# Performance work log

Hardware: AMD Instinct MI355X
Metric: run time of the kernel (lower is better)

Reference implementation:

```python
import jax, jax.numpy as jnp
import numpy as np

N_NODES = 100000
N_EDGES = 1000000
LATENT = 128
EMBED = 32


def setup_inputs() -> dict:
    key = jax.random.key(0)
    ks = jax.random.split(key, 10)
    z = jax.random.normal(ks[0], (N_NODES, LATENT), dtype=jnp.float32)
    edge_index = jax.random.randint(ks[1], (2, N_EDGES), 0, N_NODES, dtype=jnp.int64)
    bond_types = jax.random.randint(ks[2], (N_EDGES,), 0, 13, dtype=jnp.int64)
    d_in = 2 * LATENT + EMBED  # 288
    s = lambda k, shape, fan: jax.random.normal(k, shape, dtype=jnp.float32) / np.sqrt(fan)
    embed = s(ks[3], (13, EMBED), EMBED)
    W1 = s(ks[4], (d_in, LATENT), d_in)
    b1 = jnp.zeros((LATENT,), jnp.float32)
    W2 = s(ks[5], (LATENT, 64), LATENT)
    b2 = jnp.zeros((64,), jnp.float32)
    W3 = s(ks[6], (64, 1), 64)
    b3 = jnp.zeros((1,), jnp.float32)
    return {"z": z, "edge_index": edge_index, "bond_types": bond_types,
            "embed": embed, "W1": W1, "b1": b1, "W2": W2, "b2": b2,
            "W3": W3, "b3": b3}


def reference(z, edge_index, bond_types, embed, W1, b1, W2, b2, W3, b3):
    src, dst = edge_index[0], edge_index[1]
    # gather endpoint latents and bond-type embedding, concat -> [E, 288]
    features = jnp.concatenate([z[src], z[dst], embed[bond_types]], axis=-1)
    h = jax.nn.relu(features @ W1 + b1)   # dropout is identity in eval mode
    h = jax.nn.relu(h @ W2 + b2)
    out = jax.nn.softplus(h @ W3 + b3)
    return out.squeeze(-1)  # [E]
```

## Files before the change

kernel.cpp:

```cpp
#include <hip/hip_runtime.h>

#define E_EDGES 1000000
#define EBLK (E_EDGES / 64)
#define NNODES 100000
#define NGBLK ((NNODES + 63) / 64)
#define LATENT 128
#define DIN 288
#define H1DIM 128
#define PAD1 136
#define PAD2 66
#define PADA 296

#define WT1A 0
#define WT1B 16384
#define WT2S 32768
#define TPOFF 40960
#define UOFF 44288
#define UROWS 100032
#define VOFF (UOFF + UROWS * 128)
#define WS_SPLIT ((size_t)(VOFF + UROWS * 128) * 2)

#define MW1 0
#define MW2 36864

typedef __bf16 v8bf __attribute__((ext_vector_type(8)));
typedef __bf16 v4bf __attribute__((ext_vector_type(4)));
typedef __bf16 v2bf __attribute__((ext_vector_type(2)));
typedef float  v4f  __attribute__((ext_vector_type(4)));

__device__ __forceinline__ void cvt_store4(__bf16* p, float4 v) {
    v4bf o;
    o[0] = (__bf16)v.x; o[1] = (__bf16)v.y; o[2] = (__bf16)v.z; o[3] = (__bf16)v.w;
    *(v4bf*)p = o;
}


__global__ void prep_split(const float* __restrict__ W1, const float* __restrict__ W2,
                           const float* __restrict__ embed, const float* __restrict__ b1,
                           __bf16* __restrict__ ws) {
    int i = blockIdx.x * 256 + threadIdx.x;
    if (i < 16384) {
        int n = i >> 7, k = i & 127;
        ws[WT1A + i] = (__bf16)W1[k * 128 + n];
    } else if (i < 32768) {
        int idx = i - 16384;
        int n = idx >> 7, k = idx & 127;
        ws[WT1B + idx] = (__bf16)W1[(128 + k) * 128 + n];
    } else if (i < 40960) {
        int idx = i - 32768;
        int f = idx >> 7, k = idx & 127;
        ws[WT2S + idx] = (__bf16)W2[k * 64 + f];
    } else if (i < 40960 + 1664) {
        int idx = i - 40960;
        int b = idx >> 7, n = idx & 127;
        float s = b1[n];
        #pragma unroll
        for (int k = 0; k < 32; ++k)
            s += embed[b * 32 + k] * W1[(256 + k) * 128 + n];
        ((float*)(ws + TPOFF))[idx] = s;
    }
}

__global__ __launch_bounds__(256, 6) void node_gemm(
    const float* __restrict__ z, const __bf16* __restrict__ ws, __bf16* __restrict__ wsm)
{
    __shared__ __align__(16) __bf16 sA[64 * PAD1];
    const int tid = threadIdx.x;
    const int n0 = blockIdx.x * 64;

    {
        const int r = tid >> 2, j = tid & 3;
        int nd = n0 + r; if (nd >= NNODES) nd = NNODES - 1;
        const float4* zs = (const float4*)(z + (size_t)nd * LATENT);
        __bf16* rowp = &sA[r * PAD1];
        #pragma unroll
        for (int i = 0; i < 8; ++i) { int p = j + 4 * i; cvt_store4(rowp + p * 4, zs[p]); }
    }
    __syncthreads();

    const int wave = tid >> 6, lane = tid & 63, quad = lane >> 4, col16 = lane & 15;
    v4f zero4 = {0.f, 0.f, 0.f, 0.f};

    #pragma unroll
    for (int pass = 0; pass < 2; ++pass) {
        const __bf16* wt = ws + (pass == 0 ? WT1A : WT1B);
        __bf16* outp = wsm + (pass == 0 ? UOFF : VOFF) + (size_t)n0 * 128;
        const __bf16* w1p0 = wt + (size_t)(wave * 32 + 2 * col16) * 128;
        const __bf16* w1p1 = w1p0 + 128;
        v4f acc[4][2];
        #pragma unroll
        for (int mt = 0; mt < 4; ++mt) { acc[mt][0] = zero4; acc[mt][1] = zero4; }
        #pragma unroll
        for (int ks = 0; ks < 4; ++ks) {
            int k0 = ks * 32 + quad * 8;
            v8bf a0 = *(const v8bf*)&sA[(0 * 16 + col16) * PAD1 + k0];
            v8bf a1 = *(const v8bf*)&sA[(1 * 16 + col16) * PAD1 + k0];
            v8bf a2 = *(const v8bf*)&sA[(2 * 16 + col16) * PAD1 + k0];
            v8bf a3 = *(const v8bf*)&sA[(3 * 16 + col16) * PAD1 + k0];
            v8bf bb0 = *(const v8bf*)&w1p0[k0];
            v8bf bb1 = *(const v8bf*)&w1p1[k0];
            acc[0][0] = __builtin_amdgcn_mfma_f32_16x16x32_bf16(a0, bb0, acc[0][0], 0, 0, 0);
            acc[1][0] = __builtin_amdgcn_mfma_f32_16x16x32_bf16(a1, bb0, acc[1][0], 0, 0, 0);
            acc[2][0] = __builtin_amdgcn_mfma_f32_16x16x32_bf16(a2, bb0, acc[2][0], 0, 0, 0);
            acc[3][0] = __builtin_amdgcn_mfma_f32_16x16x32_bf16(a3, bb0, acc[3][0], 0, 0, 0);
            acc[0][1] = __builtin_amdgcn_mfma_f32_16x16x32_bf16(a0, bb1, acc[0][1], 0, 0, 0);
            acc[1][1] = __builtin_amdgcn_mfma_f32_16x16x32_bf16(a1, bb1, acc[1][1], 0, 0, 0);
            acc[2][1] = __builtin_amdgcn_mfma_f32_16x16x32_bf16(a2, bb1, acc[2][1], 0, 0, 0);
            acc[3][1] = __builtin_amdgcn_mfma_f32_16x16x32_bf16(a3, bb1, acc[3][1], 0, 0, 0);
        }
        #pragma unroll
        for (int mt = 0; mt < 4; ++mt) {
            #pragma unroll
            for (int rr = 0; rr < 4; ++rr) {
                int m = mt * 16 + quad * 4 + rr;
                v2bf o;
                o[0] = (__bf16)acc[mt][0][rr];
                o[1] = (__bf16)acc[mt][1][rr];
                *(v2bf*)&outp[(size_t)m * 128 + wave * 32 + 2 * col16] = o;
            }
        }
    }
}

__global__ __launch_bounds__(256, 8) void edge_kernel(
    const int* __restrict__ eidx, const int* __restrict__ bt,
    const float* __restrict__ b2, const float* __restrict__ W3,
    const float* __restrict__ b3, const __bf16* __restrict__ ws,
    float* __restrict__ out)
{
    __shared__ __align__(16) __bf16 sbuf[64 * PAD1];
    __shared__ float sb2[64];
    __shared__ float sw3[64];
    __shared__ float sb3s;
    __bf16* sH1 = sbuf;
    __bf16* sH2 = sbuf;

    const __bf16* wt2 = ws + WT2S;
    const float*  tpf = (const float*)(ws + TPOFF);
    const __bf16* U   = ws + UOFF;
    const __bf16* V   = ws + VOFF;

    const int tid = threadIdx.x;
    const int e0 = blockIdx.x * 64;

    if (tid < 64) sb2[tid] = b2[tid];
    else if (tid < 128) sw3[tid - 64] = W3[tid - 64];
    else if (tid == 128) sb3s = b3[0];

    {
        const int r = tid >> 2, j = tid & 3;
        const int e = e0 + r;
        const int isrc = __builtin_nontemporal_load(eidx + e);
        const int idst = __builtin_nontemporal_load(eidx + E_EDGES + e);
        const int ib   = __builtin_nontemporal_load(bt + e);
        const v8bf* up = (const v8bf*)(U + (size_t)isrc * 128);
        const v8bf* vp = (const v8bf*)(V + (size_t)idst * 128);
        const float4* tp = (const float4*)(tpf + ib * 128);
        __bf16* rowp = &sH1[r * PAD1];
        v8bf u[4], v[4];
        #pragma unroll
        for (int i = 0; i < 4; ++i) u[i] = up[j + 4 * i];
        #pragma unroll
        for (int i = 0; i < 4; ++i) v[i] = vp[j + 4 * i];
        #pragma unroll
        for (int i = 0; i < 4; ++i) {
            int p = j + 4 * i;
            float4 t0 = tp[p * 2], t1 = tp[p * 2 + 1];
            v8bf o;
            o[0] = (__bf16)fmaxf((float)u[i][0] + (float)v[i][0] + t0.x, 0.f);
            o[1] = (__bf16)fmaxf((float)u[i][1] + (float)v[i][1] + t0.y, 0.f);
            o[2] = (__bf16)fmaxf((float)u[i][2] + (float)v[i][2] + t0.z, 0.f);
            o[3] = (__bf16)fmaxf((float)u[i][3] + (float)v[i][3] + t0.w, 0.f);
            o[4] = (__bf16)fmaxf((float)u[i][4] + (float)v[i][4] + t1.x, 0.f);
            o[5] = (__bf16)fmaxf((float)u[i][5] + (float)v[i][5] + t1.y, 0.f);
            o[6] = (__bf16)fmaxf((float)u[i][6] + (float)v[i][6] + t1.z, 0.f);
            o[7] = (__bf16)fmaxf((float)u[i][7] + (float)v[i][7] + t1.w, 0.f);
            *(v8bf*)(rowp + p * 8) = o;
        }
    }
    __syncthreads();

    const int wave = tid >> 6, lane = tid & 63, quad = lane >> 4, col16 = lane & 15;
    v4f zero4 = {0.f, 0.f, 0.f, 0.f};

    v4f acc2[4];
    #pragma unroll
    for (int mt = 0; mt < 4; ++mt) acc2[mt] = zero4;

    const __bf16* w2p = wt2 + (size_t)(wave * 16 + col16) * H1DIM;
    #pragma unroll
    for (int ks = 0; ks < 4; ++ks) {
        int k0 = ks * 32 + quad * 8;
        v8bf bb = *(const v8bf*)&w2p[k0];
        #pragma unroll
        for (int mt = 0; mt < 4; ++mt) {
            v8bf aa = *(const v8bf*)&sH1[(mt * 16 + col16) * PAD1 + k0];
            acc2[mt] = __builtin_amdgcn_mfma_f32_16x16x32_bf16(aa, bb, acc2[mt], 0, 0, 0);
        }
    }
    __syncthreads();

    {
        int n = wave * 16 + col16;
        float bias = sb2[n];
        #pragma unroll
        for (int mt = 0; mt < 4; ++mt) {
            #pragma unroll
            for (int rr = 0; rr < 4; ++rr) {
                int m = mt * 16 + quad * 4 + rr;
                sH2[m * PAD2 + n] = (__bf16)fmaxf(acc2[mt][rr] + bias, 0.f);
            }
        }
    }
    __syncthreads();

    {
        int row = tid >> 2;
        int q   = tid & 3;
        float s = 0.f;
        #pragma unroll
        for (int kk = 0; kk < 16; ++kk) {
            int k = q * 16 + kk;
            s += (float)sH2[row * PAD2 + k] * sw3[k];
        }
        s += __shfl_xor(s, 1);
        s += __shfl_xor(s, 2);
        if (q == 0) {
            float x = s + sb3s;
            float r = fmaxf(x, 0.f) + log1pf(expf(-fabsf(x)));
            __builtin_nontemporal_store(r, out + e0 + row);
        }
    }
}


__global__ void prep_mono(const float* __restrict__ W1, const float* __restrict__ W2,
                          __bf16* __restrict__ ws) {
    int i = blockIdx.x * 256 + threadIdx.x;
    if (i < DIN * H1DIM) {
        int n = i / DIN, k = i - n * DIN;
        ws[MW1 + i] = (__bf16)W1[k * H1DIM + n];
    }
    if (i < H1DIM * 64) {
        int n = i / H1DIM, k = i - n * H1DIM;
        ws[MW2 + i] = (__bf16)W2[k * 64 + n];
    }
}

__global__ __launch_bounds__(256, 4) void fused_mono(
    const float* __restrict__ z, const int* __restrict__ eidx,
    const int* __restrict__ bt, const float* __restrict__ embed,
    const float* __restrict__ b1, const float* __restrict__ b2,
    const float* __restrict__ W3, const float* __restrict__ b3,
    const __bf16* __restrict__ ws, float* __restrict__ out)
{
    __shared__ __align__(16) __bf16 sbuf[64 * PADA];
    __shared__ __bf16 sH2[64 * PAD2];
    __shared__ float sb1[H1DIM];
    __shared__ float sb2[64];
    __shared__ float sw3[64];
    __shared__ float sb3s;
    __bf16* sA  = sbuf;
    __bf16* sH1 = sbuf;

    const __bf16* wt1 = ws + MW1;
    const __bf16* wt2 = ws + MW2;
    const int tid = threadIdx.x;
    const int e0 = blockIdx.x * 64;

    if (tid < 128) sb1[tid] = b1[tid];
    else if (tid < 192) sb2[tid - 128] = b2[tid - 128];
    else { int k = tid - 192; sw3[k] = W3[k]; if (k == 0) sb3s = b3[0]; }

    {
        const int r = tid >> 2, j = tid & 3;
        const int e = e0 + r;
        const int isrc = eidx[e];
        const int idst = eidx[E_EDGES + e];
        const int ib   = bt[e];
        const float4* zs = (const float4*)(z + (size_t)isrc * LATENT);
        const float4* zd = (const float4*)(z + (size_t)idst * LATENT);
        const float4* em = (const float4*)(embed + (size_t)ib * 32);
        __bf16* rowp = &sA[r * PADA];
        #pragma unroll
        for (int i = 0; i < 8; ++i) { int p = j + 4 * i; cvt_store4(rowp + p * 4, zs[p]); }
        #pragma unroll
        for (int i = 0; i < 8; ++i) { int p = j + 4 * i; cvt_store4(rowp + 128 + p * 4, zd[p]); }
        #pragma unroll
        for (int i = 0; i < 2; ++i) { int p = j + 4 * i; cvt_store4(rowp + 256 + p * 4, em[p]); }
    }
    __syncthreads();

    const int wave = tid >> 6, lane = tid & 63, quad = lane >> 4, col16 = lane & 15;
    v4f zero4 = {0.f, 0.f, 0.f, 0.f};
    v4f acc[4][2];
    #pragma unroll
    for (int mt = 0; mt < 4; ++mt) { acc[mt][0] = zero4; acc[mt][1] = zero4; }

    const __bf16* w1p0 = wt1 + (size_t)(wave * 32 + col16) * DIN;
    const __bf16* w1p1 = wt1 + (size_t)(wave * 32 + 16 + col16) * DIN;

    #pragma unroll
    for (int ks = 0; ks < 9; ++ks) {
        int k0 = ks * 32 + quad * 8;
        v8bf a0 = *(const v8bf*)&sA[(0 * 16 + col16) * PADA + k0];
        v8bf a1 = *(const v8bf*)&sA[(1 * 16 + col16) * PADA + k0];
        v8bf a2 = *(const v8bf*)&sA[(2 * 16 + col16) * PADA + k0];
        v8bf a3 = *(const v8bf*)&sA[(3 * 16 + col16) * PADA + k0];
        v8bf bb0 = *(const v8bf*)&w1p0[k0];
        v8bf bb1 = *(const v8bf*)&w1p1[k0];
        acc[0][0] = __builtin_amdgcn_mfma_f32_16x16x32_bf16(a0, bb0, acc[0][0], 0, 0, 0);
        acc[1][0] = __builtin_amdgcn_mfma_f32_16x16x32_bf16(a1, bb0, acc[1][0], 0, 0, 0);
        acc[2][0] = __builtin_amdgcn_mfma_f32_16x16x32_bf16(a2, bb0, acc[2][0], 0, 0, 0);
        acc[3][0] = __builtin_amdgcn_mfma_f32_16x16x32_bf16(a3, bb0, acc[3][0], 0, 0, 0);
        acc[0][1] = __builtin_amdgcn_mfma_f32_16x16x32_bf16(a0, bb1, acc[0][1], 0, 0, 0);
        acc[1][1] = __builtin_amdgcn_mfma_f32_16x16x32_bf16(a1, bb1, acc[1][1], 0, 0, 0);
        acc[2][1] = __builtin_amdgcn_mfma_f32_16x16x32_bf16(a2, bb1, acc[2][1], 0, 0, 0);
        acc[3][1] = __builtin_amdgcn_mfma_f32_16x16x32_bf16(a3, bb1, acc[3][1], 0, 0, 0);
    }
    __syncthreads();

    #pragma unroll
    for (int j = 0; j < 2; ++j) {
        int n = wave * 32 + j * 16 + col16;
        float bias = sb1[n];
        #pragma unroll
        for (int mt = 0; mt < 4; ++mt) {
            #pragma unroll
            for (int r = 0; r < 4; ++r) {
                int m = mt * 16 + quad * 4 + r;
                sH1[m * PAD1 + n] = (__bf16)fmaxf(acc[mt][j][r] + bias, 0.f);
            }
        }
    }
    __syncthreads();

    v4f acc2[4];
    #pragma unroll
    for (int mt = 0; mt < 4; ++mt) acc2[mt] = zero4;
    const __bf16* w2p = wt2 + (size_t)(wave * 16 + col16) * H1DIM;
    #pragma unroll
    for (int ks = 0; ks < 4; ++ks) {
        int k0 = ks * 32 + quad * 8;
        v8bf bb = *(const v8bf*)&w2p[k0];
        #pragma unroll
        for (int mt = 0; mt < 4; ++mt) {
            v8bf aa = *(const v8bf*)&sH1[(mt * 16 + col16) * PAD1 + k0];
            acc2[mt] = __builtin_amdgcn_mfma_f32_16x16x32_bf16(aa, bb, acc2[mt], 0, 0, 0);
        }
    }
    {
        int n = wave * 16 + col16;
        float bias = sb2[n];
        #pragma unroll
        for (int mt = 0; mt < 4; ++mt) {
            #pragma unroll
            for (int rr = 0; rr < 4; ++rr) {
                int m = mt * 16 + quad * 4 + rr;
                sH2[m * PAD2 + n] = (__bf16)fmaxf(acc2[mt][rr] + bias, 0.f);
            }
        }
    }
    __syncthreads();
    {
        int row = tid >> 2, q = tid & 3;
        float s = 0.f;
        #pragma unroll
        for (int kk = 0; kk < 16; ++kk) {
            int k = q * 16 + kk;
            s += (float)sH2[row * PAD2 + k] * sw3[k];
        }
        s += __shfl_xor(s, 1);
        s += __shfl_xor(s, 2);
        if (q == 0) {
            float x = s + sb3s;
            out[e0 + row] = fmaxf(x, 0.f) + log1pf(expf(-fabsf(x)));
        }
    }
}

extern "C" void kernel_launch(void* const* d_in, const int* in_sizes, int n_in,
                              void* d_out, int out_size, void* d_ws, size_t ws_size,
                              hipStream_t stream) {
    const float* z     = (const float*)d_in[0];
    const int*   eidx  = (const int*)d_in[1];
    const int*   btyp  = (const int*)d_in[2];
    const float* embed = (const float*)d_in[3];
    const float* W1    = (const float*)d_in[4];
    const float* b1    = (const float*)d_in[5];
    const float* W2    = (const float*)d_in[6];
    const float* b2    = (const float*)d_in[7];
    const float* W3    = (const float*)d_in[8];
    const float* b3    = (const float*)d_in[9];
    float* out = (float*)d_out;
    __bf16* ws = (__bf16*)d_ws;

    if (ws_size >= WS_SPLIT) {
        prep_split<<<167, 256, 0, stream>>>(W1, W2, embed, b1, ws);
        node_gemm<<<NGBLK, 256, 0, stream>>>(z, ws, ws);
        edge_kernel<<<EBLK, 256, 0, stream>>>(eidx, btyp, b2, W3, b3, ws, out);
    } else {
        prep_mono<<<(DIN * H1DIM + 255) / 256, 256, 0, stream>>>(W1, W2, ws);
        fused_mono<<<EBLK, 256, 0, stream>>>(z, eidx, btyp, embed,
                                             b1, b2, W3, b3, ws, out);
    }
}
```

Measured before the change: 211.9 us.

## Quantize node projections to int8 with per-row scales for edge gathers

The node GEMM now writes the U and V projections as int8 with one float scale per row. Scales come from a block-wide row max reduction, and the rows are staged through shared memory for coalesced stores. The edge kernel gathers 128-byte int8 rows plus two scales instead of 256-byte bf16 rows and dequantizes with fused multiply-adds. This halves the random gather traffic, at the cost of quantization error, extra reduction and sync work in node_gemm, and lower launch-bound occupancy there.

```diff
diff --git a/kernel.cpp b/kernel.cpp
--- a/kernel.cpp
+++ b/kernel.cpp
@@ -10,15 +10,17 @@
 #define PAD1 136
 #define PAD2 66
 #define PADA 296
+#define PADQ 144
 
 #define WT1A 0
 #define WT1B 16384
 #define WT2S 32768
 #define TPOFF 40960
-#define UOFF 44288
-#define UROWS 100032
-#define VOFF (UOFF + UROWS * 128)
-#define WS_SPLIT ((size_t)(VOFF + UROWS * 128) * 2)
+#define USCALE_E 44288
+#define VSCALE_E 244352
+#define UQ_E 444416
+#define VQ_E 6846464
+#define WS_SPLIT ((size_t)13248512 * 2)
 
 #define MW1 0
 #define MW2 36864
@@ -61,10 +63,13 @@
     }
 }
 
-__global__ __launch_bounds__(256, 6) void node_gemm(
+__global__ __launch_bounds__(256, 4) void node_gemm(
     const float* __restrict__ z, const __bf16* __restrict__ ws, __bf16* __restrict__ wsm)
 {
     __shared__ __align__(16) __bf16 sA[64 * PAD1];
+    __shared__ __align__(16) char  sQ[64 * PADQ];
+    __shared__ float smx[256];
+    __shared__ float sinvS[64];
     const int tid = threadIdx.x;
     const int n0 = blockIdx.x * 64;
 
@@ -84,7 +89,8 @@
     #pragma unroll
     for (int pass = 0; pass < 2; ++pass) {
         const __bf16* wt = ws + (pass == 0 ? WT1A : WT1B);
-        __bf16* outp = wsm + (pass == 0 ? UOFF : VOFF) + (size_t)n0 * 128;
+        signed char* qout = (signed char*)(wsm + (pass == 0 ? UQ_E : VQ_E)) + (size_t)n0 * 128;
+        float* scOut = (float*)(wsm + (pass == 0 ? USCALE_E : VSCALE_E)) + n0;
         const __bf16* w1p0 = wt + (size_t)(wave * 32 + 2 * col16) * 128;
         const __bf16* w1p1 = w1p0 + 128;
         v4f acc[4][2];
@@ -108,17 +114,62 @@
             acc[2][1] = __builtin_amdgcn_mfma_f32_16x16x32_bf16(a2, bb1, acc[2][1], 0, 0, 0);
             acc[3][1] = __builtin_amdgcn_mfma_f32_16x16x32_bf16(a3, bb1, acc[3][1], 0, 0, 0);
         }
+
+        float rmx[4][4];
+        #pragma unroll
+        for (int mt = 0; mt < 4; ++mt)
+            #pragma unroll
+            for (int rr = 0; rr < 4; ++rr)
+                rmx[mt][rr] = fmaxf(fabsf(acc[mt][0][rr]), fabsf(acc[mt][1][rr]));
+        #pragma unroll
+        for (int d = 1; d < 16; d <<= 1)
+            #pragma unroll
+            for (int mt = 0; mt < 4; ++mt)
+                #pragma unroll
+                for (int rr = 0; rr < 4; ++rr)
+                    rmx[mt][rr] = fmaxf(rmx[mt][rr], __shfl_xor(rmx[mt][rr], d));
+        if (col16 == 0) {
+            #pragma unroll
+            for (int mt = 0; mt < 4; ++mt)
+                #pragma unroll
+                for (int rr = 0; rr < 4; ++rr)
+                    smx[wave * 64 + mt * 16 + quad * 4 + rr] = rmx[mt][rr];
+        }
+        __syncthreads();
+
+        if (tid < 64) {
+            float mx = fmaxf(fmaxf(smx[tid], smx[64 + tid]),
+                             fmaxf(smx[128 + tid], smx[192 + tid]));
+            float s = 0.f, si = 0.f;
+            if (mx > 0.f) { s = mx * (1.f / 127.f); si = 127.f / mx; }
+            sinvS[tid] = si;
+            scOut[tid] = s;
+        }
+        __syncthreads();
+
         #pragma unroll
         for (int mt = 0; mt < 4; ++mt) {
             #pragma unroll
             for (int rr = 0; rr < 4; ++rr) {
                 int m = mt * 16 + quad * 4 + rr;
-                v2bf o;
-                o[0] = (__bf16)acc[mt][0][rr];
-                o[1] = (__bf16)acc[mt][1][rr];
-                *(v2bf*)&outp[(size_t)m * 128 + wave * 32 + 2 * col16] = o;
+                float si = sinvS[m];
+                int q0 = (int)rintf(acc[mt][0][rr] * si);
+                int q1 = (int)rintf(acc[mt][1][rr] * si);
+                *(unsigned short*)&sQ[m * PADQ + wave * 32 + 2 * col16] =
+                    (unsigned short)((q0 & 255) | ((q1 & 255) << 8));
             }
         }
+        __syncthreads();
+
+        {
+            #pragma unroll
+            for (int i = 0; i < 2; ++i) {
+                int idx = tid * 16 + i * 4096;
+                int m = idx >> 7, c = idx & 127;
+                *(int4*)&qout[idx] = *(const int4*)&sQ[m * PADQ + c];
+            }
+        }
+        __syncthreads();
     }
 }
 
@@ -137,8 +188,10 @@
 
     const __bf16* wt2 = ws + WT2S;
     const float*  tpf = (const float*)(ws + TPOFF);
-    const __bf16* U   = ws + UOFF;
-    const __bf16* V   = ws + VOFF;
+    const signed char* UQ = (const signed char*)(ws + UQ_E);
+    const signed char* VQ = (const signed char*)(ws + VQ_E);
+    const float* Usc = (const float*)(ws + USCALE_E);
+    const float* Vsc = (const float*)(ws + VSCALE_E);
 
     const int tid = threadIdx.x;
     const int e0 = blockIdx.x * 64;
@@ -153,29 +206,31 @@
         const int isrc = __builtin_nontemporal_load(eidx + e);
         const int idst = __builtin_nontemporal_load(eidx + E_EDGES + e);
         const int ib   = __builtin_nontemporal_load(bt + e);
-        const v8bf* up = (const v8bf*)(U + (size_t)isrc * 128);
-        const v8bf* vp = (const v8bf*)(V + (size_t)idst * 128);
-        const float4* tp = (const float4*)(tpf + ib * 128);
-        __bf16* rowp = &sH1[r * PAD1];
-        v8bf u[4], v[4];
-        #pragma unroll
-        for (int i = 0; i < 4; ++i) u[i] = up[j + 4 * i];
-        #pragma unroll
-        for (int i = 0; i < 4; ++i) v[i] = vp[j + 4 * i];
-        #pragma unroll
-        for (int i = 0; i < 4; ++i) {
-            int p = j + 4 * i;
-            float4 t0 = tp[p * 2], t1 = tp[p * 2 + 1];
+        const int4* uqp = (const int4*)(UQ + (size_t)isrc * 128);
+        const int4* vqp = (const int4*)(VQ + (size_t)idst * 128);
+        int4 uA = uqp[2 * j], uB = uqp[2 * j + 1];
+        int4 vA = vqp[2 * j], vB = vqp[2 * j + 1];
+        const float su = Usc[isrc];
+        const float sv = Vsc[idst];
+        const float4* tp = (const float4*)(tpf + ib * 128) + 8 * j;
+        __bf16* rowp = &sH1[r * PAD1] + 32 * j;
+        int uw[8] = {uA.x, uA.y, uA.z, uA.w, uB.x, uB.y, uB.z, uB.w};
+        int vw[8] = {vA.x, vA.y, vA.z, vA.w, vB.x, vB.y, vB.z, vB.w};
+        #pragma unroll
+        for (int c = 0; c < 4; ++c) {
+            float4 t0 = tp[2 * c], t1 = tp[2 * c + 1];
+            int wu0 = uw[2 * c], wu1 = uw[2 * c + 1];
+            int wv0 = vw[2 * c], wv1 = vw[2 * c + 1];
             v8bf o;
-            o[0] = (__bf16)fmaxf((float)u[i][0] + (float)v[i][0] + t0.x, 0.f);
-            o[1] = (__bf16)fmaxf((float)u[i][1] + (float)v[i][1] + t0.y, 0.f);
-            o[2] = (__bf16)fmaxf((float)u[i][2] + (float)v[i][2] + t0.z, 0.f);
-            o[3] = (__bf16)fmaxf((float)u[i][3] + (float)v[i][3] + t0.w, 0.f);
-            o[4] = (__bf16)fmaxf((float)u[i][4] + (float)v[i][4] + t1.x, 0.f);
-            o[5] = (__bf16)fmaxf((float)u[i][5] + (float)v[i][5] + t1.y, 0.f);
-            o[6] = (__bf16)fmaxf((float)u[i][6] + (float)v[i][6] + t1.z, 0.f);
-            o[7] = (__bf16)fmaxf((float)u[i][7] + (float)v[i][7] + t1.w, 0.f);
-            *(v8bf*)(rowp + p * 8) = o;
+            o[0] = (__bf16)fmaxf(fmaf(su, (float)(signed char)(wu0),       fmaf(sv, (float)(signed char)(wv0),       t0.x)), 0.f);
+            o[1] = (__bf16)fmaxf(fmaf(su, (float)(signed char)(wu0 >> 8),  fmaf(sv, (float)(signed char)(wv0 >> 8),  t0.y)), 0.f);
+            o[2] = (__bf16)fmaxf(fmaf(su, (float)(signed char)(wu0 >> 16), fmaf(sv, (float)(signed char)(wv0 >> 16), t0.z)), 0.f);
+            o[3] = (__bf16)fmaxf(fmaf(su, (float)(signed char)(wu0 >> 24), fmaf(sv, (float)(signed char)(wv0 >> 24), t0.w)), 0.f);
+            o[4] = (__bf16)fmaxf(fmaf(su, (float)(signed char)(wu1),       fmaf(sv, (float)(signed char)(wv1),       t1.x)), 0.f);
+            o[5] = (__bf16)fmaxf(fmaf(su, (float)(signed char)(wu1 >> 8),  fmaf(sv, (float)(signed char)(wv1 >> 8),  t1.y)), 0.f);
+            o[6] = (__bf16)fmaxf(fmaf(su, (float)(signed char)(wu1 >> 16), fmaf(sv, (float)(signed char)(wv1 >> 16), t1.z)), 0.f);
+            o[7] = (__bf16)fmaxf(fmaf(su, (float)(signed char)(wu1 >> 24), fmaf(sv, (float)(signed char)(wv1 >> 24), t1.w)), 0.f);
+            *(v8bf*)(rowp + 8 * c) = o;
         }
     }
     __syncthreads();
```

Result: slower. 233.6 us (+10.2%).
